# Kernel optimization log

Hardware: AMD Instinct MI355X
Metric: run time of the kernel (lower is better)

The kernel has to match this reference:

```python
import jax, jax.numpy as jnp
import numpy as np

B, S, IN_C, OUT_C = 2, 1024, 4096, 32000


def setup_inputs() -> dict:
    key = jax.random.key(0)
    k1, k2, k3 = jax.random.split(key, 3)
    hidden_states = jax.random.normal(k1, (B, S, IN_C), dtype=jnp.float32)
    weight = jax.random.normal(k2, (OUT_C, IN_C), dtype=jnp.float32) * 0.02
    bias = jax.random.normal(k3, (OUT_C,), dtype=jnp.float32) * 0.02
    return {"hidden_states": hidden_states, "weight": weight, "bias": bias,
            "split_num": 2}


def reference(hidden_states, weight, bias, split_num):
    # SlicedLMHead: split in_features into `split_num` contiguous slices,
    # run each slice as a linear to outC, accumulate, then add bias.
    in_c = hidden_states.shape[-1]
    split_size = in_c // split_num // 2 * 2
    logits = None
    for i in range(split_num):
        start = i * split_size
        end = (i + 1) * split_size if i < split_num - 1 else in_c
        h_slice = hidden_states[:, :, start:end]          # [B, S, slice]
        w_slice = weight[:, start:end]                    # [outC, slice]
        logits_slice = jnp.einsum('bsc,vc->bsv', h_slice, w_slice)
        logits = logits_slice if logits is None else logits + logits_slice
    return logits + bias
```

## Files before the change

### kernel.cpp

```cpp
#include <hip/hip_runtime.h>
#include <hip/hip_bf16.h>


typedef __attribute__((ext_vector_type(8))) short bhalf8;
typedef __attribute__((ext_vector_type(4))) float f32x4;
typedef __attribute__((ext_vector_type(8))) unsigned short us8;

#define M_DIM 2048
#define N_DIM 32000
#define K_DIM 4096
#define BM 256
#define BN 256
#define BK 64
#define NT (K_DIM / BK)
#define MBLKS (M_DIM / BM)
#define NBLKS (N_DIM / BN)
#define NWG (MBLKS * NBLKS)

#define W_ELEMS ((size_t)N_DIM * K_DIM)
#define H_ELEMS ((size_t)M_DIM * K_DIM)
#define WS_NEEDED ((W_ELEMS + H_ELEMS) * 2)

#define GLOAD_LDS16(g, l) \
    __builtin_amdgcn_global_load_lds( \
        (const __attribute__((address_space(1))) unsigned int*)(g), \
        (__attribute__((address_space(3))) unsigned int*)(l), 16, 0, 0)

__device__ __forceinline__ unsigned short f2bf_rn(float f) {
    unsigned int u = __float_as_uint(f);
    u += 0x7FFFu + ((u >> 16) & 1u);
    return (unsigned short)(u >> 16);
}

__global__ __launch_bounds__(256)
void cvt_f32_bf16(const float* __restrict__ in, unsigned short* __restrict__ out,
                  size_t n8) {
    size_t i = (size_t)blockIdx.x * blockDim.x + threadIdx.x;
    const size_t stride = (size_t)gridDim.x * blockDim.x;
    for (; i < n8; i += stride) {
        const float4 v0 = ((const float4*)in)[i * 2];
        const float4 v1 = ((const float4*)in)[i * 2 + 1];
        us8 p;
        p[0] = f2bf_rn(v0.x); p[1] = f2bf_rn(v0.y);
        p[2] = f2bf_rn(v0.z); p[3] = f2bf_rn(v0.w);
        p[4] = f2bf_rn(v1.x); p[5] = f2bf_rn(v1.y);
        p[6] = f2bf_rn(v1.z); p[7] = f2bf_rn(v1.w);
        ((us8*)out)[i] = p;
    }
}

__global__ __launch_bounds__(512, 2)
void lmhead_gemm_256(const unsigned short* __restrict__ A,
                     const unsigned short* __restrict__ W,
                     const float* __restrict__ bias,
                     float* __restrict__ C)
{
    __shared__ unsigned short lds[65536];

    const int tid  = threadIdx.x;
    const int bid  = blockIdx.x;
    const int wgid = (bid & 7) * (NWG / 8) + (bid >> 3);
    const int mblk = wgid & (MBLKS - 1);
    const int nblk = wgid >> 3;

    const int lane = tid & 63;
    const int wv   = tid >> 6;
    const int wr   = wv >> 2;
    const int wc   = wv & 3;
    const int l15  = lane & 15;
    const int l4   = lane >> 4;

    const int strow = tid >> 3;
    const int sgsw  = ((tid & 7) ^ (strow & 7)) << 3;
    const unsigned short* const srcA = A + (size_t)(mblk * BM + strow) * K_DIM + sgsw;
    const unsigned short* const srcB = W + (size_t)(nblk * BN + strow) * K_DIM + sgsw;
    const int dstw = (tid & 448) * 8;

#define STAGE_A(u, h, BUF) { \
        const unsigned short* s_ = srcA + (size_t)((h) * 128) * K_DIM + (size_t)(u) * BK; \
        unsigned short* d_ = &lds[(((BUF) * 2 + (h)) * 8192) + dstw]; \
        GLOAD_LDS16(s_, d_); GLOAD_LDS16(s_ + (size_t)64 * K_DIM, d_ + 4096); }
#define STAGE_B(u, h, BUF) { \
        const unsigned short* s_ = srcB + (size_t)((h) * 128) * K_DIM + (size_t)(u) * BK; \
        unsigned short* d_ = &lds[32768 + (((BUF) * 2 + (h)) * 8192) + dstw]; \
        GLOAD_LDS16(s_, d_); GLOAD_LDS16(s_ + (size_t)64 * K_DIM, d_ + 4096); }

    const int swz0 = (l4 ^ (l15 & 7)) << 3;
    const int swz1 = ((4 + l4) ^ (l15 & 7)) << 3;
    const int arow = l15 * 64;
    const int brow = ((wc & 1) * 64 + l15) * 64;

    f32x4 acc[8][4] = {};
    bhalf8 af0[4][2], af1[4][2], bf01[2][2], bf23[2][2];

#define READ_AF0(BUF) { \
        const unsigned short* _as = &lds[((BUF) * 2 + wr) * 8192]; \
        _Pragma("unroll") \
        for (int i = 0; i < 4; ++i) { \
            af0[i][0] = *(const bhalf8*)&_as[arow + swz0 + i * 1024]; \
            af0[i][1] = *(const bhalf8*)&_as[arow + swz1 + i * 1024]; } }
#define READ_AF1(BUF) { \
        const unsigned short* _as = &lds[((BUF) * 2 + wr) * 8192]; \
        _Pragma("unroll") \
        for (int i = 0; i < 4; ++i) { \
            af1[i][0] = *(const bhalf8*)&_as[arow + swz0 + 4096 + i * 1024]; \
            af1[i][1] = *(const bhalf8*)&_as[arow + swz1 + 4096 + i * 1024]; } }
#define READ_BF01(BUF) { \
        const unsigned short* _bs = &lds[32768 + ((BUF) * 2 + (wc >> 1)) * 8192]; \
        _Pragma("unroll") \
        for (int j = 0; j < 2; ++j) { \
            bf01[j][0] = *(const bhalf8*)&_bs[brow + swz0 + j * 1024]; \
            bf01[j][1] = *(const bhalf8*)&_bs[brow + swz1 + j * 1024]; } }
#define READ_BF23(BUF) { \
        const unsigned short* _bs = &lds[32768 + ((BUF) * 2 + (wc >> 1)) * 8192]; \
        _Pragma("unroll") \
        for (int j = 0; j < 2; ++j) { \
            bf23[j][0] = *(const bhalf8*)&_bs[brow + swz0 + (2 + j) * 1024]; \
            bf23[j][1] = *(const bhalf8*)&_bs[brow + swz1 + (2 + j) * 1024]; } }

#define MFMA8Q(AF, BF, IOFF, JOFF) { \
        _Pragma("unroll") \
        for (int i = 0; i < 4; ++i) \
            _Pragma("unroll") \
            for (int j = 0; j < 2; ++j) \
                _Pragma("unroll") \
                for (int kk = 0; kk < 2; ++kk) \
                    acc[(IOFF) + i][(JOFF) + j] = __builtin_amdgcn_mfma_f32_16x16x32_bf16( \
                        AF[i][kk], BF[j][kk], acc[(IOFF) + i][(JOFF) + j], 0, 0, 0); }

#define SBAR  __builtin_amdgcn_sched_barrier(0)
#define BARR  __builtin_amdgcn_s_barrier()
#define LGKM(n) asm volatile("s_waitcnt lgkmcnt(" #n ")" ::: "memory")
#define VMC(n)  asm volatile("s_waitcnt vmcnt(" #n ")" ::: "memory")
#define PRIO1 __builtin_amdgcn_s_setprio(1)
#define PRIO0 __builtin_amdgcn_s_setprio(0)

    STAGE_A(0, 0, 0); STAGE_A(0, 1, 0);
    STAGE_B(0, 0, 0); STAGE_B(0, 1, 0);
    STAGE_B(1, 0, 1); STAGE_B(1, 1, 1);
    SBAR;
    VMC(4);
    SBAR;
    BARR;
    READ_AF0(0); READ_BF01(0);
    SBAR;

    #pragma unroll 1
    for (int s2 = 0; s2 < NT; s2 += 2) {
        const int T1 = s2 + 1;
        const bool m2 = (s2 + 2) < NT;

        READ_BF23(0); STAGE_A(T1, 0, 1); SBAR;
        BARR; LGKM(4); SBAR;
        PRIO1; MFMA8Q(af0, bf01, 0, 0); PRIO0; SBAR;
        BARR;
        READ_AF1(0); STAGE_A(T1, 1, 1); SBAR;
        BARR; LGKM(8); SBAR;
        PRIO1; MFMA8Q(af0, bf23, 0, 2); PRIO0; SBAR;
        BARR;
        if (m2) STAGE_B(s2 + 2, 0, 0);
        SBAR;
        BARR; LGKM(0); SBAR;
        PRIO1; MFMA8Q(af1, bf01, 4, 0); PRIO0; SBAR;
        if (m2) { VMC(2); } else { VMC(0); }
        SBAR;
        BARR;
        READ_AF0(1); READ_BF01(1);
        if (m2) STAGE_B(s2 + 2, 1, 0);
        SBAR;
        BARR; SBAR;
        PRIO1; MFMA8Q(af1, bf23, 4, 2); PRIO0; SBAR;
        BARR;
        READ_BF23(1);
        if (m2) STAGE_A(s2 + 2, 0, 0);
        SBAR;
        BARR; LGKM(4); SBAR;
        PRIO1; MFMA8Q(af0, bf01, 0, 0); PRIO0; SBAR;
        BARR;
        READ_AF1(1);
        if (m2) STAGE_A(s2 + 2, 1, 0);
        SBAR;
        BARR; LGKM(8); SBAR;
        PRIO1; MFMA8Q(af0, bf23, 0, 2); PRIO0; SBAR;
        BARR;
        if (m2) STAGE_B(T1 + 2, 0, 1);
        SBAR;
        BARR; LGKM(0); SBAR;
        PRIO1; MFMA8Q(af1, bf01, 4, 0); PRIO0; SBAR;
        if (m2) { VMC(2); } else { VMC(0); }
        SBAR;
        BARR;
        if (m2) { READ_AF0(0); READ_BF01(0); }
        if (m2) STAGE_B(T1 + 2, 1, 1);
        SBAR;
        BARR; SBAR;
        PRIO1; MFMA8Q(af1, bf23, 4, 2); PRIO0; SBAR;
        BARR;
    }

    const size_t crow0 = (size_t)(mblk * BM + wr * 128 + l4 * 4);
    const int    ccol0 = nblk * BN + wc * 64 + l15;
    #pragma unroll
    for (int j = 0; j < 4; ++j) {
        const float bv = bias[ccol0 + j * 16];
        #pragma unroll
        for (int i = 0; i < 8; ++i) {
            const size_t base = (crow0 + (size_t)i * 16) * N_DIM + ccol0 + j * 16;
            #pragma unroll
            for (int r = 0; r < 4; ++r)
                C[base + (size_t)r * N_DIM] = acc[i][j][r] + bv;
        }
    }
#undef STAGE_A
#undef STAGE_B
#undef READ_AF0
#undef READ_AF1
#undef READ_BF01
#undef READ_BF23
#undef MFMA8Q
#undef SBAR
#undef BARR
#undef LGKM
#undef VMC
#undef PRIO1
#undef PRIO0
}

__global__ __launch_bounds__(256, 2)
void lmhead_gemm_f32(const float* __restrict__ A, const float* __restrict__ W,
                     const float* __restrict__ bias, float* __restrict__ C) {
    __shared__ unsigned short As[2][128 * 64];
    __shared__ unsigned short Bs[2][128 * 64];

    const int tid  = threadIdx.x;
    const int bid  = blockIdx.x;
    const int mblk = bid & 15;
    const int nblk = bid >> 4;
    const int st_row = tid >> 3;
    const int st_g   = tid & 7;
    const int lane = tid & 63;
    const int wv   = tid >> 6;
    const int wm   = (wv >> 1) << 6;
    const int wn   = (wv & 1) << 6;
    const int l15  = lane & 15;
    const int l4   = lane >> 4;

    const float* aptr = A + (size_t)(mblk * 128 + st_row) * K_DIM + st_g * 8;
    const float* bptr = W + (size_t)(nblk * 128 + st_row) * K_DIM + st_g * 8;

    f32x4 acc[4][4] = {};
    float4 ra[4][2], rb[4][2];

    #pragma unroll
    for (int s = 0; s < 4; ++s) {
        const float* ap = aptr + (size_t)(s * 32) * K_DIM;
        const float* bp = bptr + (size_t)(s * 32) * K_DIM;
        ra[s][0] = *(const float4*)(ap);   ra[s][1] = *(const float4*)(ap + 4);
        rb[s][0] = *(const float4*)(bp);   rb[s][1] = *(const float4*)(bp + 4);
    }
    #pragma unroll
    for (int s = 0; s < 4; ++s) {
        const int row = s * 32 + st_row;
        const int off = row * 64 + ((st_g ^ (row & 7)) << 3);
        us8 pa, pb;
        #pragma unroll
        for (int j = 0; j < 4; ++j) {
            pa[j] = f2bf_rn(((const float*)&ra[s][0])[j]);
            pa[j + 4] = f2bf_rn(((const float*)&ra[s][1])[j]);
            pb[j] = f2bf_rn(((const float*)&rb[s][0])[j]);
            pb[j + 4] = f2bf_rn(((const float*)&rb[s][1])[j]);
        }
        *(us8*)&As[0][off] = pa;  *(us8*)&Bs[0][off] = pb;
    }
    __syncthreads();

    for (int t = 0; t < 64; ++t) {
        const int cur = t & 1;
        const bool more = (t + 1) < 64;
        if (more) {
            const float* ap = aptr + (size_t)(t + 1) * 64;
            const float* bp = bptr + (size_t)(t + 1) * 64;
            #pragma unroll
            for (int s = 0; s < 4; ++s) {
                ra[s][0] = *(const float4*)(ap + (size_t)(s * 32) * K_DIM);
                ra[s][1] = *(const float4*)(ap + (size_t)(s * 32) * K_DIM + 4);
                rb[s][0] = *(const float4*)(bp + (size_t)(s * 32) * K_DIM);
                rb[s][1] = *(const float4*)(bp + (size_t)(s * 32) * K_DIM + 4);
            }
        }
        const unsigned short* as = As[cur];
        const unsigned short* bs = Bs[cur];
        #pragma unroll
        for (int kk = 0; kk < 2; ++kk) {
            bhalf8 af[4], bfv[4];
            #pragma unroll
            for (int mf = 0; mf < 4; ++mf) {
                const int row = wm + mf * 16 + l15;
                af[mf] = *(const bhalf8*)&as[row * 64 + ((((kk << 2) + l4) ^ (row & 7)) << 3)];
            }
            #pragma unroll
            for (int nf = 0; nf < 4; ++nf) {
                const int row = wn + nf * 16 + l15;
                bfv[nf] = *(const bhalf8*)&bs[row * 64 + ((((kk << 2) + l4) ^ (row & 7)) << 3)];
            }
            #pragma unroll
            for (int mf = 0; mf < 4; ++mf)
                #pragma unroll
                for (int nf = 0; nf < 4; ++nf)
                    acc[mf][nf] = __builtin_amdgcn_mfma_f32_16x16x32_bf16(
                        af[mf], bfv[nf], acc[mf][nf], 0, 0, 0);
        }
        if (more) {
            const int nbuf = cur ^ 1;
            #pragma unroll
            for (int s = 0; s < 4; ++s) {
                const int row = s * 32 + st_row;
                const int off = row * 64 + ((st_g ^ (row & 7)) << 3);
                us8 pa, pb;
                #pragma unroll
                for (int j = 0; j < 4; ++j) {
                    pa[j] = f2bf_rn(((const float*)&ra[s][0])[j]);
                    pa[j + 4] = f2bf_rn(((const float*)&ra[s][1])[j]);
                    pb[j] = f2bf_rn(((const float*)&rb[s][0])[j]);
                    pb[j + 4] = f2bf_rn(((const float*)&rb[s][1])[j]);
                }
                *(us8*)&As[nbuf][off] = pa;  *(us8*)&Bs[nbuf][off] = pb;
            }
        }
        __syncthreads();
    }

    const size_t crow0 = (size_t)(mblk * 128 + wm + l4 * 4);
    const int    ccol0 = nblk * 128 + wn + l15;
    #pragma unroll
    for (int nf = 0; nf < 4; ++nf) {
        const float bv = bias[ccol0 + nf * 16];
        #pragma unroll
        for (int mf = 0; mf < 4; ++mf) {
            const size_t base = (crow0 + (size_t)mf * 16) * N_DIM + ccol0 + nf * 16;
            #pragma unroll
            for (int r = 0; r < 4; ++r)
                C[base + (size_t)r * N_DIM] = acc[mf][nf][r] + bv;
        }
    }
}

extern "C" void kernel_launch(void* const* d_in, const int* in_sizes, int n_in,
                              void* d_out, int out_size, void* d_ws, size_t ws_size,
                              hipStream_t stream) {
    const float* h = (const float*)d_in[0];
    const float* w = (const float*)d_in[1];
    const float* b = (const float*)d_in[2];
    float* out = (float*)d_out;

    if (ws_size >= WS_NEEDED) {
        unsigned short* wbf = (unsigned short*)d_ws;
        unsigned short* hbf = wbf + W_ELEMS;
        cvt_f32_bf16<<<2048, 256, 0, stream>>>(w, wbf, W_ELEMS / 8);
        cvt_f32_bf16<<<512, 256, 0, stream>>>(h, hbf, H_ELEMS / 8);
        lmhead_gemm_256<<<NWG, 512, 0, stream>>>(hbf, wbf, b, out);
    } else {
        lmhead_gemm_f32<<<4000, 256, 0, stream>>>(h, w, b, out);
    }
}
```

Before: 622.3 us.

## Pre-pack bf16 operands into MFMA fragment order during conversion

The f32-to-bf16 conversion kernels now write H and W in a blocked layout that matches the order of the MFMA fragments, so each 16-byte chunk sits where a lane will later read it. The GEMM stages contiguous 8 KB blocks into LDS with linear addressing and reads fragments at lane*8 offsets, which removes the XOR swizzle arithmetic and the strided global loads. In exchange, the conversion kernels do strided row reads of the f32 inputs with scattered 16-byte writes, which may hurt conversion bandwidth. LDS bank conflicts could also reappear, because the reads are now unswizzled.

```diff
diff --git a/kernel.cpp b/kernel.cpp
--- a/kernel.cpp
+++ b/kernel.cpp
@@ -33,25 +33,63 @@
 }
 
 __global__ __launch_bounds__(256)
-void cvt_f32_bf16(const float* __restrict__ in, unsigned short* __restrict__ out,
-                  size_t n8) {
-    size_t i = (size_t)blockIdx.x * blockDim.x + threadIdx.x;
-    const size_t stride = (size_t)gridDim.x * blockDim.x;
-    for (; i < n8; i += stride) {
-        const float4 v0 = ((const float4*)in)[i * 2];
-        const float4 v1 = ((const float4*)in)[i * 2 + 1];
+void cvt_w_frag(const float* __restrict__ w, unsigned short* __restrict__ wn) {
+    const int lane = threadIdx.x & 63;
+    const int nwav = gridDim.x * 4;
+    const int l15  = lane & 15;
+    const int l4g  = (lane >> 4) * 8;
+    for (int c = blockIdx.x * 4 + (threadIdx.x >> 6); c < 256000; c += nwav) {
+        const int f   = c & 15;
+        const int t   = (c >> 4) & 63;
+        const int hh  = (c >> 10) & 1;
+        const int nb  = c >> 11;
+        const int kk  = f & 1;
+        const int j   = (f >> 1) & 3;
+        const int wcb = f >> 3;
+        const int row = nb * 256 + hh * 128 + wcb * 64 + j * 16 + l15;
+        const int k   = t * 64 + kk * 32 + l4g;
+        const float* s = w + (size_t)row * K_DIM + k;
+        const float4 v0 = *(const float4*)s;
+        const float4 v1 = *(const float4*)(s + 4);
         us8 p;
         p[0] = f2bf_rn(v0.x); p[1] = f2bf_rn(v0.y);
         p[2] = f2bf_rn(v0.z); p[3] = f2bf_rn(v0.w);
         p[4] = f2bf_rn(v1.x); p[5] = f2bf_rn(v1.y);
         p[6] = f2bf_rn(v1.z); p[7] = f2bf_rn(v1.w);
-        ((us8*)out)[i] = p;
+        *(us8*)(wn + (size_t)c * 512 + lane * 8) = p;
+    }
+}
+
+__global__ __launch_bounds__(256)
+void cvt_h_frag(const float* __restrict__ h, unsigned short* __restrict__ hn) {
+    const int lane = threadIdx.x & 63;
+    const int nwav = gridDim.x * 4;
+    const int l15  = lane & 15;
+    const int l4g  = (lane >> 4) * 8;
+    for (int c = blockIdx.x * 4 + (threadIdx.x >> 6); c < 16384; c += nwav) {
+        const int f  = c & 15;
+        const int t  = (c >> 4) & 63;
+        const int hh = (c >> 10) & 1;
+        const int mb = c >> 11;
+        const int kk = f & 1;
+        const int i  = f >> 1;
+        const int row = mb * 256 + hh * 128 + i * 16 + l15;
+        const int k   = t * 64 + kk * 32 + l4g;
+        const float* s = h + (size_t)row * K_DIM + k;
+        const float4 v0 = *(const float4*)s;
+        const float4 v1 = *(const float4*)(s + 4);
+        us8 p;
+        p[0] = f2bf_rn(v0.x); p[1] = f2bf_rn(v0.y);
+        p[2] = f2bf_rn(v0.z); p[3] = f2bf_rn(v0.w);
+        p[4] = f2bf_rn(v1.x); p[5] = f2bf_rn(v1.y);
+        p[6] = f2bf_rn(v1.z); p[7] = f2bf_rn(v1.w);
+        *(us8*)(hn + (size_t)c * 512 + lane * 8) = p;
     }
 }
 
 __global__ __launch_bounds__(512, 2)
-void lmhead_gemm_256(const unsigned short* __restrict__ A,
-                     const unsigned short* __restrict__ W,
+void lmhead_gemm_256(const unsigned short* __restrict__ Hf,
+                     const unsigned short* __restrict__ Wf,
                      const float* __restrict__ bias,
                      float* __restrict__ C)
 {
@@ -70,53 +108,44 @@
     const int l15  = lane & 15;
     const int l4   = lane >> 4;
 
-    const int strow = tid >> 3;
-    const int sgsw  = ((tid & 7) ^ (strow & 7)) << 3;
-    const unsigned short* const srcA = A + (size_t)(mblk * BM + strow) * K_DIM + sgsw;
-    const unsigned short* const srcB = W + (size_t)(nblk * BN + strow) * K_DIM + sgsw;
     const int dstw = (tid & 448) * 8;
 
 #define STAGE_A(u, h, BUF) { \
-        const unsigned short* s_ = srcA + (size_t)((h) * 128) * K_DIM + (size_t)(u) * BK; \
+        const unsigned short* s_ = Hf + ((size_t)((mblk * 2 + (h)) * 64 + (u))) * 8192 + tid * 8; \
         unsigned short* d_ = &lds[(((BUF) * 2 + (h)) * 8192) + dstw]; \
-        GLOAD_LDS16(s_, d_); GLOAD_LDS16(s_ + (size_t)64 * K_DIM, d_ + 4096); }
+        GLOAD_LDS16(s_, d_); GLOAD_LDS16(s_ + 4096, d_ + 4096); }
 #define STAGE_B(u, h, BUF) { \
-        const unsigned short* s_ = srcB + (size_t)((h) * 128) * K_DIM + (size_t)(u) * BK; \
+        const unsigned short* s_ = Wf + ((size_t)((nblk * 2 + (h)) * 64 + (u))) * 8192 + tid * 8; \
         unsigned short* d_ = &lds[32768 + (((BUF) * 2 + (h)) * 8192) + dstw]; \
-        GLOAD_LDS16(s_, d_); GLOAD_LDS16(s_ + (size_t)64 * K_DIM, d_ + 4096); }
-
-    const int swz0 = (l4 ^ (l15 & 7)) << 3;
-    const int swz1 = ((4 + l4) ^ (l15 & 7)) << 3;
-    const int arow = l15 * 64;
-    const int brow = ((wc & 1) * 64 + l15) * 64;
+        GLOAD_LDS16(s_, d_); GLOAD_LDS16(s_ + 4096, d_ + 4096); }
 
     f32x4 acc[8][4] = {};
     bhalf8 af0[4][2], af1[4][2], bf01[2][2], bf23[2][2];
 
 #define READ_AF0(BUF) { \
-        const unsigned short* _as = &lds[((BUF) * 2 + wr) * 8192]; \
+        const unsigned short* _as = &lds[((BUF) * 2 + wr) * 8192 + lane * 8]; \
         _Pragma("unroll") \
         for (int i = 0; i < 4; ++i) { \
-            af0[i][0] = *(const bhalf8*)&_as[arow + swz0 + i * 1024]; \
-            af0[i][1] = *(const bhalf8*)&_as[arow + swz1 + i * 1024]; } }
+            af0[i][0] = *(const bhalf8*)&_as[(i * 2 + 0) * 512]; \
+            af0[i][1] = *(const bhalf8*)&_as[(i * 2 + 1) * 512]; } }
 #define READ_AF1(BUF) { \
-        const unsigned short* _as = &lds[((BUF) * 2 + wr) * 8192]; \
+        const unsigned short* _as = &lds[((BUF) * 2 + wr) * 8192 + lane * 8]; \
         _Pragma("unroll") \
         for (int i = 0; i < 4; ++i) { \
-            af1[i][0] = *(const bhalf8*)&_as[arow + swz0 + 4096 + i * 1024]; \
-            af1[i][1] = *(const bhalf8*)&_as[arow + swz1 + 4096 + i * 1024]; } }
+            af1[i][0] = *(const bhalf8*)&_as[((4 + i) * 2 + 0) * 512]; \
+            af1[i][1] = *(const bhalf8*)&_as[((4 + i) * 2 + 1) * 512]; } }
 #define READ_BF01(BUF) { \
-        const unsigned short* _bs = &lds[32768 + ((BUF) * 2 + (wc >> 1)) * 8192]; \
+        const unsigned short* _bs = &lds[32768 + ((BUF) * 2 + (wc >> 1)) * 8192 + (wc & 1) * 4096 + lane * 8]; \
         _Pragma("unroll") \
         for (int j = 0; j < 2; ++j) { \
-            bf01[j][0] = *(const bhalf8*)&_bs[brow + swz0 + j * 1024]; \
-            bf01[j][1] = *(const bhalf8*)&_bs[brow + swz1 + j * 1024]; } }
+            bf01[j][0] = *(const bhalf8*)&_bs[(j * 2 + 0) * 512]; \
+            bf01[j][1] = *(const bhalf8*)&_bs[(j * 2 + 1) * 512]; } }
 #define READ_BF23(BUF) { \
-        const unsigned short* _bs = &lds[32768 + ((BUF) * 2 + (wc >> 1)) * 8192]; \
+        const unsigned short* _bs = &lds[32768 + ((BUF) * 2 + (wc >> 1)) * 8192 + (wc & 1) * 4096 + lane * 8]; \
         _Pragma("unroll") \
         for (int j = 0; j < 2; ++j) { \
-            bf23[j][0] = *(const bhalf8*)&_bs[brow + swz0 + (2 + j) * 1024]; \
-            bf23[j][1] = *(const bhalf8*)&_bs[brow + swz1 + (2 + j) * 1024]; } }
+            bf23[j][0] = *(const bhalf8*)&_bs[((2 + j) * 2 + 0) * 512]; \
+            bf23[j][1] = *(const bhalf8*)&_bs[((2 + j) * 2 + 1) * 512]; } }
 
 #define MFMA8Q(AF, BF, IOFF, JOFF) { \
         _Pragma("unroll") \
@@ -356,8 +385,8 @@
     if (ws_size >= WS_NEEDED) {
         unsigned short* wbf = (unsigned short*)d_ws;
         unsigned short* hbf = wbf + W_ELEMS;
-        cvt_f32_bf16<<<2048, 256, 0, stream>>>(w, wbf, W_ELEMS / 8);
-        cvt_f32_bf16<<<512, 256, 0, stream>>>(h, hbf, H_ELEMS / 8);
+        cvt_w_frag<<<2048, 256, 0, stream>>>(w, wbf);
+        cvt_h_frag<<<2048, 256, 0, stream>>>(h, hbf);
         lmhead_gemm_256<<<NWG, 512, 0, stream>>>(hbf, wbf, b, out);
     } else {
         lmhead_gemm_f32<<<4000, 256, 0, stream>>>(h, w, b, out);
```

New measurement: 631.0 us. About the same (+1.4%).
